# Kernel optimization log

Hardware: AMD Instinct MI355X
Metric: run time of the kernel (lower is better)

## Reference

```python
import jax, jax.numpy as jnp
import numpy as np

N = 6144
IN_DIM = 256
OUT_DIM = 256
NUM_HEADS = 4
HEAD_DIM = OUT_DIM // NUM_HEADS  # 64
NEG_SLOPE = 0.2


def setup_inputs() -> dict:
    key = jax.random.key(0)
    k_x, k_adj, k_W, k_a = jax.random.split(key, 4)
    x = jax.random.normal(k_x, (N, IN_DIM), dtype=jnp.float32)
    adj = jax.random.randint(k_adj, (N, N), 0, 2, dtype=jnp.int32)
    # nn.Linear(in_dim, out_dim, bias=False): store as [in_dim, out_dim] so y = x @ W
    W = jax.random.normal(k_W, (IN_DIM, OUT_DIM), dtype=jnp.float32) / np.sqrt(IN_DIM)
    # nn.Linear(2*head_dim, 1, bias=False): a single attention vector shared across heads
    a = jax.random.normal(k_a, (2 * HEAD_DIM,), dtype=jnp.float32) / np.sqrt(2 * HEAD_DIM)
    return {"x": x, "adj": adj, "W": W, "a": a}


def reference(x, adj, W, a):
    n = x.shape[0]
    Wh = (x @ W).reshape(n, NUM_HEADS, HEAD_DIM)  # (N, H, D)
    a_src, a_dst = a[:HEAD_DIM], a[HEAD_DIM:]
    # score[h,i,j] = leaky_relu(a_src . Wh[i,h] + a_dst . Wh[j,h])
    f_src = jnp.einsum('nhd,d->hn', Wh, a_src)  # (H, N)
    f_dst = jnp.einsum('nhd,d->hn', Wh, a_dst)  # (H, N)
    e = f_src[:, :, None] + f_dst[:, None, :]   # (H, N, N)
    e = jnp.where(e > 0, e, NEG_SLOPE * e)      # LeakyReLU(0.2)
    mask = (adj != 0)[None, :, :]               # (1, N, N)
    e = jnp.where(mask, e, -jnp.inf)
    alpha = jax.nn.softmax(e, axis=-1)          # (H, N, N)
    alpha = jnp.nan_to_num(alpha, nan=0.0)      # empty rows -> 0 (matches torch)
    # dropout: eval mode (identity)
    out = jnp.einsum('hij,jhd->ihd', alpha, Wh).reshape(n, OUT_DIM)
    return out
```

## Files before the change

### kernel.cpp

```cpp
#include <hip/hip_runtime.h>

#define NN 6144
#define SHIFTC (12.0f*1.4426950408889634f)
#define LOG2E 1.4426950408889634f

typedef float f32x4 __attribute__((ext_vector_type(4)));
typedef short short8 __attribute__((ext_vector_type(8)));
typedef int   i32x4 __attribute__((ext_vector_type(4)));

__device__ __forceinline__ float bf2f(unsigned short u){
  return __uint_as_float(((unsigned int)u)<<16);
}
__device__ __forceinline__ unsigned short f2bf(float f){
  unsigned int x = __float_as_uint(f);
  x += 0x7fffu + ((x>>16)&1u);
  return (unsigned short)(x>>16);
}

__global__ __launch_bounds__(256) void k_gemm(const float* __restrict__ x,
                                              const float* __restrict__ W,
                                              unsigned short* __restrict__ wht){
  __shared__ float sx[16*256];
  const int t = threadIdx.x;
  const int i0 = blockIdx.x * 16;
  {
    const int r = t >> 4, kc = t & 15;
    const float* src = x + (size_t)(i0 + r)*256 + kc*16;
    float* dst = sx + r*256 + kc*16;
#pragma unroll
    for (int q = 0; q < 4; ++q)
      *reinterpret_cast<f32x4*>(dst + 4*q) = *reinterpret_cast<const f32x4*>(src + 4*q);
  }
  __syncthreads();
  float acc[16];
#pragma unroll
  for (int r = 0; r < 16; ++r) acc[r] = 0.f;
  for (int k = 0; k < 256; k += 4) {
    const float w0 = W[(size_t)(k+0)*256 + t];
    const float w1 = W[(size_t)(k+1)*256 + t];
    const float w2 = W[(size_t)(k+2)*256 + t];
    const float w3 = W[(size_t)(k+3)*256 + t];
#pragma unroll
    for (int r = 0; r < 16; ++r) {
      f32x4 xv = *reinterpret_cast<const f32x4*>(sx + r*256 + k);
      acc[r] = fmaf(xv.x, w0, acc[r]);
      acc[r] = fmaf(xv.y, w1, acc[r]);
      acc[r] = fmaf(xv.z, w2, acc[r]);
      acc[r] = fmaf(xv.w, w3, acc[r]);
    }
  }
  alignas(16) unsigned short buf[16];
#pragma unroll
  for (int r = 0; r < 16; ++r) buf[r] = f2bf(acc[r]);
  unsigned short* dst = wht + (size_t)t*NN + i0;
  *reinterpret_cast<uint4*>(dst)     = *reinterpret_cast<const uint4*>(buf);
  *reinterpret_cast<uint4*>(dst + 8) = *reinterpret_cast<const uint4*>(buf + 8);
}

__global__ __launch_bounds__(256) void k_f(const unsigned short* __restrict__ wht,
                                           const float* __restrict__ a,
                                           float* __restrict__ fs2,
                                           float* __restrict__ edp,
                                           float* __restrict__ edn){
  __shared__ unsigned short sw[256*64];
  const int t = threadIdx.x;
  const int i0 = blockIdx.x * 64;
  {
    const unsigned short* src = wht + (size_t)t*NN + i0;
    unsigned short* dst = sw + t*64;
#pragma unroll
    for (int q = 0; q < 8; ++q)
      *reinterpret_cast<uint4*>(dst + q*8) = *reinterpret_cast<const uint4*>(src + q*8);
  }
  __syncthreads();
  const int ii = t & 63, h = t >> 6;
  float s_ = 0.f, d_ = 0.f;
#pragma unroll 16
  for (int d = 0; d < 64; ++d) {
    const float v = bf2f(sw[(h*64 + d)*64 + ii]);
    s_ = fmaf(v, a[d],      s_);
    d_ = fmaf(v, a[64 + d], d_);
  }
  const float fs2v = s_ * LOG2E;
  const float fd2v = d_ * LOG2E;
  fs2[(size_t)h*NN + i0 + ii] = fs2v;
  edp[(size_t)h*NN + i0 + ii] = exp2f(fd2v - SHIFTC);
  edn[(size_t)h*NN + i0 + ii] = exp2f(0.2f * fd2v);
}

__global__ __launch_bounds__(256) void k_attn(const int* __restrict__ adj,
                                              const unsigned short* __restrict__ wht,
                                              const float* __restrict__ fs2,
                                              const float* __restrict__ edp,
                                              const float* __restrict__ edn,
                                              float* __restrict__ apart,
                                              float* __restrict__ lpart,
                                              int nsteps){
  __shared__ unsigned short swht[2][64*72];
  __shared__ unsigned int   smask[2][128];
  __shared__ float          sedp[2][64];
  __shared__ float          sedn[2][64];
  const int t  = threadIdx.x;
  const int w  = t >> 6, l = t & 63, lr = l & 15, hi = l >> 4;
  const int bid = blockIdx.x;
  const int h   = (bid >> 3) & 3;
  const int g   = (bid & 7) | ((bid >> 5) << 3);
  const int it  = g % 96;
  const int js  = g / 96;
  const int i0 = it * 64;
  const int jbase = js * nsteps * 64;
  const int i_row = i0 + w*16 + lr;

  const float fsv  = fs2[(size_t)h*NN + i_row];
  const float EiNh = exp2f(-0.8f*fsv - SHIFTC);

  f32x4 acc[4];
#pragma unroll
  for (int q = 0; q < 4; ++q) acc[q] = (f32x4){0.f,0.f,0.f,0.f};
  float ls = 0.f;

  const int r_ = t >> 2, ch_ = t & 3;
  const int* asrc = adj + (size_t)(i0 + r_)*NN + jbase + ch_*16;
  const unsigned short* wsrc = wht + (size_t)(h*64 + r_)*NN + jbase + ch_*16;
  const float* pesrc = edp + (size_t)h*NN + jbase;
  const float* nesrc = edn + (size_t)h*NN + jbase;

  {
    i32x4 aj[4];
#pragma unroll
    for (int q = 0; q < 4; ++q) aj[q] = *reinterpret_cast<const i32x4*>(asrc + q*4);
    const uint4 wv0 = *reinterpret_cast<const uint4*>(wsrc);
    const uint4 wv1 = *reinterpret_cast<const uint4*>(wsrc + 8);
    unsigned int bits = 0u;
#pragma unroll
    for (int q = 0; q < 4; ++q) {
      bits |= ((unsigned)aj[q].x) << (q*4 + 0);
      bits |= ((unsigned)aj[q].y) << (q*4 + 1);
      bits |= ((unsigned)aj[q].z) << (q*4 + 2);
      bits |= ((unsigned)aj[q].w) << (q*4 + 3);
    }
    unsigned short* dst = &swht[0][r_*72 + ch_*16];
    *reinterpret_cast<uint4*>(dst)     = wv0;
    *reinterpret_cast<uint4*>(dst + 8) = wv1;
    reinterpret_cast<unsigned short*>(smask[0])[r_*4 + ch_] = (unsigned short)bits;
    if (t < 64) { sedp[0][t] = pesrc[t]; sedn[0][t] = nesrc[t]; }
  }
  __syncthreads();

  for (int st = 0; st < nsteps; ++st) {
    const int cur = st & 1, nxt = cur ^ 1;
    const bool pf = (st + 1) < nsteps;

    i32x4 ajp[4]; uint4 wvp0, wvp1; float pep = 0.f, nep = 0.f;
    if (pf) {
      const int o = (st + 1) * 64;
#pragma unroll
      for (int q = 0; q < 4; ++q)
        ajp[q] = *reinterpret_cast<const i32x4*>(asrc + o + q*4);
      wvp0 = *reinterpret_cast<const uint4*>(wsrc + o);
      wvp1 = *reinterpret_cast<const uint4*>(wsrc + o + 8);
      if (t < 64) { pep = pesrc[o + t]; nep = nesrc[o + t]; }
    }

    const unsigned int m0 = smask[cur][(w*16 + lr)*2 + 0];
    const unsigned int m1 = smask[cur][(w*16 + lr)*2 + 1];
    float maskf[16];
#pragma unroll
    for (int e = 0; e < 8; ++e) {
      maskf[e]     = ((m0 >> (8*hi + e)) & 1u) ? 1.f : 0.f;
      maskf[8 + e] = ((m1 >> (8*hi + e)) & 1u) ? 1.f : 0.f;
    }
    const f32x4 ep0 = *reinterpret_cast<const f32x4*>(&sedp[cur][8*hi + 0]);
    const f32x4 ep1 = *reinterpret_cast<const f32x4*>(&sedp[cur][8*hi + 4]);
    const f32x4 ep2 = *reinterpret_cast<const f32x4*>(&sedp[cur][32 + 8*hi + 0]);
    const f32x4 ep3 = *reinterpret_cast<const f32x4*>(&sedp[cur][32 + 8*hi + 4]);
    const f32x4 en0 = *reinterpret_cast<const f32x4*>(&sedn[cur][8*hi + 0]);
    const f32x4 en1 = *reinterpret_cast<const f32x4*>(&sedn[cur][8*hi + 4]);
    const f32x4 en2 = *reinterpret_cast<const f32x4*>(&sedn[cur][32 + 8*hi + 0]);
    const f32x4 en3 = *reinterpret_cast<const f32x4*>(&sedn[cur][32 + 8*hi + 4]);
    float p[16];
#pragma unroll
    for (int e = 0; e < 4; ++e) {
      p[e]      = maskf[e]      * fmaxf(ep0[e], EiNh * en0[e]);
      p[4 + e]  = maskf[4 + e]  * fmaxf(ep1[e], EiNh * en1[e]);
      p[8 + e]  = maskf[8 + e]  * fmaxf(ep2[e], EiNh * en2[e]);
      p[12 + e] = maskf[12 + e] * fmaxf(ep3[e], EiNh * en3[e]);
    }
    float lsh = 0.f;
#pragma unroll
    for (int e = 0; e < 16; ++e) lsh += p[e];
    ls += lsh;
    int4 aw0, aw1;
    asm("v_cvt_pk_bf16_f32 %0, %1, %2" : "=v"(aw0.x) : "v"(p[0]),  "v"(p[1]));
    asm("v_cvt_pk_bf16_f32 %0, %1, %2" : "=v"(aw0.y) : "v"(p[2]),  "v"(p[3]));
    asm("v_cvt_pk_bf16_f32 %0, %1, %2" : "=v"(aw0.z) : "v"(p[4]),  "v"(p[5]));
    asm("v_cvt_pk_bf16_f32 %0, %1, %2" : "=v"(aw0.w) : "v"(p[6]),  "v"(p[7]));
    asm("v_cvt_pk_bf16_f32 %0, %1, %2" : "=v"(aw1.x) : "v"(p[8]),  "v"(p[9]));
    asm("v_cvt_pk_bf16_f32 %0, %1, %2" : "=v"(aw1.y) : "v"(p[10]), "v"(p[11]));
    asm("v_cvt_pk_bf16_f32 %0, %1, %2" : "=v"(aw1.z) : "v"(p[12]), "v"(p[13]));
    asm("v_cvt_pk_bf16_f32 %0, %1, %2" : "=v"(aw1.w) : "v"(p[14]), "v"(p[15]));
    const short8 af0 = __builtin_bit_cast(short8, aw0);
    const short8 af1 = __builtin_bit_cast(short8, aw1);
#pragma unroll
    for (int nc = 0; nc < 4; ++nc) {
      const unsigned short* bp = &swht[cur][(nc*16 + lr)*72 + 8*hi];
      const short8 b0 = *reinterpret_cast<const short8*>(bp);
      const short8 b1 = *reinterpret_cast<const short8*>(bp + 32);
      acc[nc] = __builtin_amdgcn_mfma_f32_16x16x32_bf16(af0, b0, acc[nc], 0, 0, 0);
      acc[nc] = __builtin_amdgcn_mfma_f32_16x16x32_bf16(af1, b1, acc[nc], 0, 0, 0);
    }

    if (pf) {
      unsigned int bits = 0u;
#pragma unroll
      for (int q = 0; q < 4; ++q) {
        bits |= ((unsigned)ajp[q].x) << (q*4 + 0);
        bits |= ((unsigned)ajp[q].y) << (q*4 + 1);
        bits |= ((unsigned)ajp[q].z) << (q*4 + 2);
        bits |= ((unsigned)ajp[q].w) << (q*4 + 3);
      }
      unsigned short* dst = &swht[nxt][r_*72 + ch_*16];
      *reinterpret_cast<uint4*>(dst)     = wvp0;
      *reinterpret_cast<uint4*>(dst + 8) = wvp1;
      reinterpret_cast<unsigned short*>(smask[nxt])[r_*4 + ch_] = (unsigned short)bits;
      if (t < 64) { sedp[nxt][t] = pep; sedn[nxt][t] = nep; }
    }
    __syncthreads();
  }

  {
    float v = ls;
    v += __shfl_xor(v, 16, 64);
    v += __shfl_xor(v, 32, 64);
    ls = v;
  }
  if (hi == 0)
    lpart[((size_t)js*4 + h)*NN + i_row] = ls;
#pragma unroll
  for (int nc = 0; nc < 4; ++nc)
#pragma unroll
    for (int rg = 0; rg < 4; ++rg) {
      const int irow = i0 + w*16 + 4*hi + rg;
      const int col  = h*64 + nc*16 + lr;
      apart[((size_t)js*NN + irow)*256 + col] = acc[nc][rg];
    }
}

__global__ __launch_bounds__(256) void k_comb(const float* __restrict__ apart,
                                              const float* __restrict__ lpart,
                                              float* __restrict__ out,
                                              int jsplit){
  const int idx = blockIdx.x * 256 + threadIdx.x;
  const int i = idx >> 8, c = idx & 255, h = c >> 6;
  float num = 0.f, den = 0.f;
  for (int s = 0; s < jsplit; ++s) {
    num += apart[((size_t)s*NN + i)*256 + c];
    den += lpart[((size_t)s*4 + h)*NN + i];
  }
  out[idx] = (den > 0.f) ? (num / den) : 0.f;
}

extern "C" void kernel_launch(void* const* d_in, const int* in_sizes, int n_in,
                              void* d_out, int out_size, void* d_ws, size_t ws_size,
                              hipStream_t stream) {
  const float* x   = (const float*)d_in[0];
  const int*   adj = (const int*)d_in[1];
  const float* W   = (const float*)d_in[2];
  const float* a   = (const float*)d_in[3];
  float* out = (float*)d_out;
  char* ws = (char*)d_ws;

  size_t off = 0;
  unsigned short* wht = (unsigned short*)(ws + off); off += (size_t)256*NN*2;
  float* fs2 = (float*)(ws + off); off += (size_t)4*NN*4;
  float* edp = (float*)(ws + off); off += (size_t)4*NN*4;
  float* edn = (float*)(ws + off); off += (size_t)4*NN*4;

  int jsplit = 8;
  while (jsplit > 1 &&
         off + (size_t)jsplit*4*NN*4 + (size_t)jsplit*NN*256*4 > ws_size)
    jsplit >>= 1;

  float* lpart = (float*)(ws + off); off += (size_t)jsplit*4*NN*4;
  float* apart = (float*)(ws + off);

  const int nsteps = NN / (jsplit * 64);

  k_gemm<<<dim3(NN/16), dim3(256), 0, stream>>>(x, W, wht);
  k_f   <<<dim3(NN/64), dim3(256), 0, stream>>>(wht, a, fs2, edp, edn);
  k_attn<<<dim3(4*(NN/64)*jsplit), dim3(256), 0, stream>>>(adj, wht, fs2, edp, edn, apart, lpart, nsteps);
  k_comb<<<dim3((out_size + 255)/256), dim3(256), 0, stream>>>(apart, lpart, out, jsplit);
}
```

Baseline: 113.4 us.

## Prefetch adjacency two steps ahead and compute softmax denominator via MFMA

Restructures the main loop into a manually unrolled two-stage ping-pong. Adjacency loads are issued two steps ahead while the bf16 features and edge terms are loaded one step ahead, so global-load latency overlaps more MFMA work. The per-row sum of probabilities now comes from an extra MFMA against a ones vector instead of a scalar add chain and cross-lane shuffles. The edp/edn loads are also split across two thread groups. In exchange it uses more registers and two extra MFMAs per step, and the denominator is now summed from bf16-rounded values, matching the numerator.

```diff
diff --git a/kernel.cpp b/kernel.cpp
--- a/kernel.cpp
+++ b/kernel.cpp
@@ -117,7 +117,9 @@
   f32x4 acc[4];
 #pragma unroll
   for (int q = 0; q < 4; ++q) acc[q] = (f32x4){0.f,0.f,0.f,0.f};
-  float ls = 0.f;
+  f32x4 acc_den = (f32x4){0.f,0.f,0.f,0.f};
+  const short8 vones = { (short)0x3F80,(short)0x3F80,(short)0x3F80,(short)0x3F80,
+                         (short)0x3F80,(short)0x3F80,(short)0x3F80,(short)0x3F80 };
 
   const int r_ = t >> 2, ch_ = t & 3;
   const int* asrc = adj + (size_t)(i0 + r_)*NN + jbase + ch_*16;
@@ -125,50 +127,29 @@
   const float* pesrc = edp + (size_t)h*NN + jbase;
   const float* nesrc = edn + (size_t)h*NN + jbase;
 
-  {
-    i32x4 aj[4];
-#pragma unroll
-    for (int q = 0; q < 4; ++q) aj[q] = *reinterpret_cast<const i32x4*>(asrc + q*4);
-    const uint4 wv0 = *reinterpret_cast<const uint4*>(wsrc);
-    const uint4 wv1 = *reinterpret_cast<const uint4*>(wsrc + 8);
-    unsigned int bits = 0u;
-#pragma unroll
-    for (int q = 0; q < 4; ++q) {
-      bits |= ((unsigned)aj[q].x) << (q*4 + 0);
-      bits |= ((unsigned)aj[q].y) << (q*4 + 1);
-      bits |= ((unsigned)aj[q].z) << (q*4 + 2);
-      bits |= ((unsigned)aj[q].w) << (q*4 + 3);
-    }
-    unsigned short* dst = &swht[0][r_*72 + ch_*16];
-    *reinterpret_cast<uint4*>(dst)     = wv0;
-    *reinterpret_cast<uint4*>(dst + 8) = wv1;
-    reinterpret_cast<unsigned short*>(smask[0])[r_*4 + ch_] = (unsigned short)bits;
-    if (t < 64) { sedp[0][t] = pesrc[t]; sedn[0][t] = nesrc[t]; }
-  }
-  __syncthreads();
-
-  for (int st = 0; st < nsteps; ++st) {
-    const int cur = st & 1, nxt = cur ^ 1;
-    const bool pf = (st + 1) < nsteps;
-
-    i32x4 ajp[4]; uint4 wvp0, wvp1; float pep = 0.f, nep = 0.f;
-    if (pf) {
-      const int o = (st + 1) * 64;
-#pragma unroll
-      for (int q = 0; q < 4; ++q)
-        ajp[q] = *reinterpret_cast<const i32x4*>(asrc + o + q*4);
-      wvp0 = *reinterpret_cast<const uint4*>(wsrc + o);
-      wvp1 = *reinterpret_cast<const uint4*>(wsrc + o + 8);
-      if (t < 64) { pep = pesrc[o + t]; nep = nesrc[o + t]; }
-    }
-
+  auto commit = [&](int nxt, i32x4 A0, i32x4 A1, i32x4 A2, i32x4 A3,
+                    uint4 W0, uint4 W1, float PE, float NE) {
+    unsigned int bits =
+        ((unsigned)A0.x)       | (((unsigned)A0.y)<<1)  | (((unsigned)A0.z)<<2)  | (((unsigned)A0.w)<<3)  |
+        (((unsigned)A1.x)<<4)  | (((unsigned)A1.y)<<5)  | (((unsigned)A1.z)<<6)  | (((unsigned)A1.w)<<7)  |
+        (((unsigned)A2.x)<<8)  | (((unsigned)A2.y)<<9)  | (((unsigned)A2.z)<<10) | (((unsigned)A2.w)<<11) |
+        (((unsigned)A3.x)<<12) | (((unsigned)A3.y)<<13) | (((unsigned)A3.z)<<14) | (((unsigned)A3.w)<<15);
+    unsigned short* dst = &swht[nxt][r_*72 + ch_*16];
+    *reinterpret_cast<uint4*>(dst)     = W0;
+    *reinterpret_cast<uint4*>(dst + 8) = W1;
+    reinterpret_cast<unsigned short*>(smask[nxt])[r_*4 + ch_] = (unsigned short)bits;
+    if (t < 64)       sedp[nxt][t]      = PE;
+    else if (t < 128) sedn[nxt][t - 64] = NE;
+  };
+
+  auto compute_step = [&](int cur) {
     const unsigned int m0 = smask[cur][(w*16 + lr)*2 + 0];
     const unsigned int m1 = smask[cur][(w*16 + lr)*2 + 1];
     float maskf[16];
 #pragma unroll
     for (int e = 0; e < 8; ++e) {
-      maskf[e]     = ((m0 >> (8*hi + e)) & 1u) ? 1.f : 0.f;
-      maskf[8 + e] = ((m1 >> (8*hi + e)) & 1u) ? 1.f : 0.f;
+      maskf[e]     = (float)((m0 >> (8*hi + e)) & 1u);
+      maskf[8 + e] = (float)((m1 >> (8*hi + e)) & 1u);
     }
     const f32x4 ep0 = *reinterpret_cast<const f32x4*>(&sedp[cur][8*hi + 0]);
     const f32x4 ep1 = *reinterpret_cast<const f32x4*>(&sedp[cur][8*hi + 4]);
@@ -186,10 +167,6 @@
       p[8 + e]  = maskf[8 + e]  * fmaxf(ep2[e], EiNh * en2[e]);
       p[12 + e] = maskf[12 + e] * fmaxf(ep3[e], EiNh * en3[e]);
     }
-    float lsh = 0.f;
-#pragma unroll
-    for (int e = 0; e < 16; ++e) lsh += p[e];
-    ls += lsh;
     int4 aw0, aw1;
     asm("v_cvt_pk_bf16_f32 %0, %1, %2" : "=v"(aw0.x) : "v"(p[0]),  "v"(p[1]));
     asm("v_cvt_pk_bf16_f32 %0, %1, %2" : "=v"(aw0.y) : "v"(p[2]),  "v"(p[3]));
@@ -201,6 +178,8 @@
     asm("v_cvt_pk_bf16_f32 %0, %1, %2" : "=v"(aw1.w) : "v"(p[14]), "v"(p[15]));
     const short8 af0 = __builtin_bit_cast(short8, aw0);
     const short8 af1 = __builtin_bit_cast(short8, aw1);
+    acc_den = __builtin_amdgcn_mfma_f32_16x16x32_bf16(af0, vones, acc_den, 0, 0, 0);
+    acc_den = __builtin_amdgcn_mfma_f32_16x16x32_bf16(af1, vones, acc_den, 0, 0, 0);
 #pragma unroll
     for (int nc = 0; nc < 4; ++nc) {
       const unsigned short* bp = &swht[cur][(nc*16 + lr)*72 + 8*hi];
@@ -209,33 +188,73 @@
       acc[nc] = __builtin_amdgcn_mfma_f32_16x16x32_bf16(af0, b0, acc[nc], 0, 0, 0);
       acc[nc] = __builtin_amdgcn_mfma_f32_16x16x32_bf16(af1, b1, acc[nc], 0, 0, 0);
     }
-
-    if (pf) {
-      unsigned int bits = 0u;
-#pragma unroll
-      for (int q = 0; q < 4; ++q) {
-        bits |= ((unsigned)ajp[q].x) << (q*4 + 0);
-        bits |= ((unsigned)ajp[q].y) << (q*4 + 1);
-        bits |= ((unsigned)ajp[q].z) << (q*4 + 2);
-        bits |= ((unsigned)ajp[q].w) << (q*4 + 3);
-      }
-      unsigned short* dst = &swht[nxt][r_*72 + ch_*16];
-      *reinterpret_cast<uint4*>(dst)     = wvp0;
-      *reinterpret_cast<uint4*>(dst + 8) = wvp1;
-      reinterpret_cast<unsigned short*>(smask[nxt])[r_*4 + ch_] = (unsigned short)bits;
-      if (t < 64) { sedp[nxt][t] = pep; sedn[nxt][t] = nep; }
+  };
+
+  i32x4 ajA0, ajA1, ajA2, ajA3, ajB0, ajB1, ajB2, ajB3;
+  {
+    const i32x4 a0 = *reinterpret_cast<const i32x4*>(asrc + 0);
+    const i32x4 a1 = *reinterpret_cast<const i32x4*>(asrc + 4);
+    const i32x4 a2 = *reinterpret_cast<const i32x4*>(asrc + 8);
+    const i32x4 a3 = *reinterpret_cast<const i32x4*>(asrc + 12);
+    const uint4 w0 = *reinterpret_cast<const uint4*>(wsrc);
+    const uint4 w1 = *reinterpret_cast<const uint4*>(wsrc + 8);
+    const float pe = (t < 64) ? pesrc[t] : 0.f;
+    const float ne = (t >= 64 && t < 128) ? nesrc[t - 64] : 0.f;
+    commit(0, a0, a1, a2, a3, w0, w1, pe, ne);
+  }
+  if (nsteps > 1) {
+    const int* an = asrc + 64;
+    ajA0 = *reinterpret_cast<const i32x4*>(an + 0);
+    ajA1 = *reinterpret_cast<const i32x4*>(an + 4);
+    ajA2 = *reinterpret_cast<const i32x4*>(an + 8);
+    ajA3 = *reinterpret_cast<const i32x4*>(an + 12);
+  }
+  __syncthreads();
+
+  for (int st = 0; st < nsteps; st += 2) {
+    if (st + 2 < nsteps) {
+      const int* an = asrc + (st + 2)*64;
+      ajB0 = *reinterpret_cast<const i32x4*>(an + 0);
+      ajB1 = *reinterpret_cast<const i32x4*>(an + 4);
+      ajB2 = *reinterpret_cast<const i32x4*>(an + 8);
+      ajB3 = *reinterpret_cast<const i32x4*>(an + 12);
+    }
+    {
+      const int o = (st + 1)*64;
+      const uint4 wv0 = *reinterpret_cast<const uint4*>(wsrc + o);
+      const uint4 wv1 = *reinterpret_cast<const uint4*>(wsrc + o + 8);
+      const float pe = (t < 64) ? pesrc[o + t] : 0.f;
+      const float ne = (t >= 64 && t < 128) ? nesrc[o + t - 64] : 0.f;
+      compute_step(0);
+      commit(1, ajA0, ajA1, ajA2, ajA3, wv0, wv1, pe, ne);
     }
     __syncthreads();
-  }
-
-  {
-    float v = ls;
-    v += __shfl_xor(v, 16, 64);
-    v += __shfl_xor(v, 32, 64);
-    ls = v;
-  }
-  if (hi == 0)
-    lpart[((size_t)js*4 + h)*NN + i_row] = ls;
+    if (st + 3 < nsteps) {
+      const int* an = asrc + (st + 3)*64;
+      ajA0 = *reinterpret_cast<const i32x4*>(an + 0);
+      ajA1 = *reinterpret_cast<const i32x4*>(an + 4);
+      ajA2 = *reinterpret_cast<const i32x4*>(an + 8);
+      ajA3 = *reinterpret_cast<const i32x4*>(an + 12);
+    }
+    if (st + 2 < nsteps) {
+      const int o = (st + 2)*64;
+      const uint4 wv0 = *reinterpret_cast<const uint4*>(wsrc + o);
+      const uint4 wv1 = *reinterpret_cast<const uint4*>(wsrc + o + 8);
+      const float pe = (t < 64) ? pesrc[o + t] : 0.f;
+      const float ne = (t >= 64 && t < 128) ? nesrc[o + t - 64] : 0.f;
+      compute_step(1);
+      commit(0, ajB0, ajB1, ajB2, ajB3, wv0, wv1, pe, ne);
+    } else {
+      compute_step(1);
+    }
+    __syncthreads();
+  }
+
+  if (lr == 0) {
+#pragma unroll
+    for (int rg = 0; rg < 4; ++rg)
+      lpart[((size_t)js*4 + h)*NN + i0 + w*16 + 4*hi + rg] = acc_den[rg];
+  }
 #pragma unroll
   for (int nc = 0; nc < 4; ++nc)
 #pragma unroll
```

Result: slower. 128.1 us (+12.9%).

## Widen attention j-tile to 128 with two wave groups and LDS reduction

Applied to the files above, without the earlier changes.

The attention kernel now uses 512 threads per block and processes a 128-wide j tile each step. Two groups of four waves each handle half of the columns and combine their partial accumulators and row sums through shared memory at the end. This halves the number of loop iterations and block-wide barriers per block and gives more waves to hide memory latency. In exchange it uses more LDS and registers per block, which may lower occupancy, and it adds a reduction pass at the end.

```diff
diff --git a/kernel.cpp b/kernel.cpp
--- a/kernel.cpp
+++ b/kernel.cpp
@@ -1,6 +1,8 @@
 #include <hip/hip_runtime.h>
 
 #define NN 6144
+#define BK 128
+#define WPAD 136
 #define SHIFTC (12.0f*1.4426950408889634f)
 #define LOG2E 1.4426950408889634f
 
@@ -88,7 +90,7 @@
   edn[(size_t)h*NN + i0 + ii] = exp2f(0.2f * fd2v);
 }
 
-__global__ __launch_bounds__(256) void k_attn(const int* __restrict__ adj,
+__global__ __launch_bounds__(512) void k_attn(const int* __restrict__ adj,
                                               const unsigned short* __restrict__ wht,
                                               const float* __restrict__ fs2,
                                               const float* __restrict__ edp,
@@ -96,20 +98,22 @@
                                               float* __restrict__ apart,
                                               float* __restrict__ lpart,
                                               int nsteps){
-  __shared__ unsigned short swht[2][64*72];
-  __shared__ unsigned int   smask[2][128];
-  __shared__ float          sedp[2][64];
-  __shared__ float          sedn[2][64];
+  __shared__ unsigned short swht[2][64*WPAD];
+  __shared__ unsigned int   smask[2][256];
+  __shared__ float          sedp[2][BK];
+  __shared__ float          sedn[2][BK];
   const int t  = threadIdx.x;
-  const int w  = t >> 6, l = t & 63, lr = l & 15, hi = l >> 4;
+  const int w8 = t >> 6, l = t & 63, lr = l & 15, hi = l >> 4;
+  const int ww = w8 & 3;
+  const int jh = w8 >> 2;
   const int bid = blockIdx.x;
   const int h   = (bid >> 3) & 3;
   const int g   = (bid & 7) | ((bid >> 5) << 3);
   const int it  = g % 96;
   const int js  = g / 96;
   const int i0 = it * 64;
-  const int jbase = js * nsteps * 64;
-  const int i_row = i0 + w*16 + lr;
+  const int jbase = js * nsteps * BK;
+  const int i_row = i0 + ww*16 + lr;
 
   const float fsv  = fs2[(size_t)h*NN + i_row];
   const float EiNh = exp2f(-0.8f*fsv - SHIFTC);
@@ -119,7 +123,7 @@
   for (int q = 0; q < 4; ++q) acc[q] = (f32x4){0.f,0.f,0.f,0.f};
   float ls = 0.f;
 
-  const int r_ = t >> 2, ch_ = t & 3;
+  const int r_ = t >> 3, ch_ = t & 7;
   const int* asrc = adj + (size_t)(i0 + r_)*NN + jbase + ch_*16;
   const unsigned short* wsrc = wht + (size_t)(h*64 + r_)*NN + jbase + ch_*16;
   const float* pesrc = edp + (size_t)h*NN + jbase;
@@ -139,11 +143,12 @@
       bits |= ((unsigned)aj[q].z) << (q*4 + 2);
       bits |= ((unsigned)aj[q].w) << (q*4 + 3);
     }
-    unsigned short* dst = &swht[0][r_*72 + ch_*16];
+    unsigned short* dst = &swht[0][r_*WPAD + ch_*16];
     *reinterpret_cast<uint4*>(dst)     = wv0;
     *reinterpret_cast<uint4*>(dst + 8) = wv1;
-    reinterpret_cast<unsigned short*>(smask[0])[r_*4 + ch_] = (unsigned short)bits;
-    if (t < 64) { sedp[0][t] = pesrc[t]; sedn[0][t] = nesrc[t]; }
+    reinterpret_cast<unsigned short*>(smask[0])[r_*8 + ch_] = (unsigned short)bits;
+    if (t < BK)          sedp[0][t]      = pesrc[t];
+    else if (t < 2*BK)   sedn[0][t - BK] = nesrc[t - BK];
   }
   __syncthreads();
 
@@ -153,31 +158,34 @@
 
     i32x4 ajp[4]; uint4 wvp0, wvp1; float pep = 0.f, nep = 0.f;
     if (pf) {
-      const int o = (st + 1) * 64;
+      const int o = (st + 1) * BK;
 #pragma unroll
       for (int q = 0; q < 4; ++q)
         ajp[q] = *reinterpret_cast<const i32x4*>(asrc + o + q*4);
       wvp0 = *reinterpret_cast<const uint4*>(wsrc + o);
       wvp1 = *reinterpret_cast<const uint4*>(wsrc + o + 8);
-      if (t < 64) { pep = pesrc[o + t]; nep = nesrc[o + t]; }
-    }
-
-    const unsigned int m0 = smask[cur][(w*16 + lr)*2 + 0];
-    const unsigned int m1 = smask[cur][(w*16 + lr)*2 + 1];
+      if (t < BK)        pep = pesrc[o + t];
+      else if (t < 2*BK) nep = nesrc[o + t - BK];
+    }
+
+    const int row = ww*16 + lr;
+    const unsigned int m0 = smask[cur][row*4 + jh*2 + 0];
+    const unsigned int m1 = smask[cur][row*4 + jh*2 + 1];
     float maskf[16];
 #pragma unroll
     for (int e = 0; e < 8; ++e) {
-      maskf[e]     = ((m0 >> (8*hi + e)) & 1u) ? 1.f : 0.f;
-      maskf[8 + e] = ((m1 >> (8*hi + e)) & 1u) ? 1.f : 0.f;
-    }
-    const f32x4 ep0 = *reinterpret_cast<const f32x4*>(&sedp[cur][8*hi + 0]);
-    const f32x4 ep1 = *reinterpret_cast<const f32x4*>(&sedp[cur][8*hi + 4]);
-    const f32x4 ep2 = *reinterpret_cast<const f32x4*>(&sedp[cur][32 + 8*hi + 0]);
-    const f32x4 ep3 = *reinterpret_cast<const f32x4*>(&sedp[cur][32 + 8*hi + 4]);
-    const f32x4 en0 = *reinterpret_cast<const f32x4*>(&sedn[cur][8*hi + 0]);
-    const f32x4 en1 = *reinterpret_cast<const f32x4*>(&sedn[cur][8*hi + 4]);
-    const f32x4 en2 = *reinterpret_cast<const f32x4*>(&sedn[cur][32 + 8*hi + 0]);
-    const f32x4 en3 = *reinterpret_cast<const f32x4*>(&sedn[cur][32 + 8*hi + 4]);
+      maskf[e]     = (float)((m0 >> (8*hi + e)) & 1u);
+      maskf[8 + e] = (float)((m1 >> (8*hi + e)) & 1u);
+    }
+    const int jo = jh*64;
+    const f32x4 ep0 = *reinterpret_cast<const f32x4*>(&sedp[cur][jo + 8*hi + 0]);
+    const f32x4 ep1 = *reinterpret_cast<const f32x4*>(&sedp[cur][jo + 8*hi + 4]);
+    const f32x4 ep2 = *reinterpret_cast<const f32x4*>(&sedp[cur][jo + 32 + 8*hi + 0]);
+    const f32x4 ep3 = *reinterpret_cast<const f32x4*>(&sedp[cur][jo + 32 + 8*hi + 4]);
+    const f32x4 en0 = *reinterpret_cast<const f32x4*>(&sedn[cur][jo + 8*hi + 0]);
+    const f32x4 en1 = *reinterpret_cast<const f32x4*>(&sedn[cur][jo + 8*hi + 4]);
+    const f32x4 en2 = *reinterpret_cast<const f32x4*>(&sedn[cur][jo + 32 + 8*hi + 0]);
+    const f32x4 en3 = *reinterpret_cast<const f32x4*>(&sedn[cur][jo + 32 + 8*hi + 4]);
     float p[16];
 #pragma unroll
     for (int e = 0; e < 4; ++e) {
@@ -203,7 +211,7 @@
     const short8 af1 = __builtin_bit_cast(short8, aw1);
 #pragma unroll
     for (int nc = 0; nc < 4; ++nc) {
-      const unsigned short* bp = &swht[cur][(nc*16 + lr)*72 + 8*hi];
+      const unsigned short* bp = &swht[cur][(nc*16 + lr)*WPAD + jo + 8*hi];
       const short8 b0 = *reinterpret_cast<const short8*>(bp);
       const short8 b1 = *reinterpret_cast<const short8*>(bp + 32);
       acc[nc] = __builtin_amdgcn_mfma_f32_16x16x32_bf16(af0, b0, acc[nc], 0, 0, 0);
@@ -219,31 +227,52 @@
         bits |= ((unsigned)ajp[q].z) << (q*4 + 2);
         bits |= ((unsigned)ajp[q].w) << (q*4 + 3);
       }
-      unsigned short* dst = &swht[nxt][r_*72 + ch_*16];
+      unsigned short* dst = &swht[nxt][r_*WPAD + ch_*16];
       *reinterpret_cast<uint4*>(dst)     = wvp0;
       *reinterpret_cast<uint4*>(dst + 8) = wvp1;
-      reinterpret_cast<unsigned short*>(smask[nxt])[r_*4 + ch_] = (unsigned short)bits;
-      if (t < 64) { sedp[nxt][t] = pep; sedn[nxt][t] = nep; }
+      reinterpret_cast<unsigned short*>(smask[nxt])[r_*8 + ch_] = (unsigned short)bits;
+      if (t < BK)        sedp[nxt][t]      = pep;
+      else if (t < 2*BK) sedn[nxt][t - BK] = nep;
     }
     __syncthreads();
   }
 
-  {
-    float v = ls;
-    v += __shfl_xor(v, 16, 64);
-    v += __shfl_xor(v, 32, 64);
-    ls = v;
-  }
-  if (hi == 0)
-    lpart[((size_t)js*4 + h)*NN + i_row] = ls;
-#pragma unroll
-  for (int nc = 0; nc < 4; ++nc)
-#pragma unroll
-    for (int rg = 0; rg < 4; ++rg) {
-      const int irow = i0 + w*16 + 4*hi + rg;
-      const int col  = h*64 + nc*16 + lr;
-      apart[((size_t)js*NN + irow)*256 + col] = acc[nc][rg];
-    }
+  float* scr = reinterpret_cast<float*>(swht);
+  const int sbase = (ww*64 + l) * 17;
+  if (jh == 1) {
+#pragma unroll
+    for (int nc = 0; nc < 4; ++nc)
+#pragma unroll
+      for (int rg = 0; rg < 4; ++rg)
+        scr[sbase + nc*4 + rg] = acc[nc][rg];
+    scr[sbase + 16] = ls;
+  }
+  __syncthreads();
+  if (jh == 0) {
+#pragma unroll
+    for (int nc = 0; nc < 4; ++nc)
+#pragma unroll
+      for (int rg = 0; rg < 4; ++rg)
+        acc[nc][rg] += scr[sbase + nc*4 + rg];
+    ls += scr[sbase + 16];
+
+    {
+      float v = ls;
+      v += __shfl_xor(v, 16, 64);
+      v += __shfl_xor(v, 32, 64);
+      ls = v;
+    }
+    if (hi == 0)
+      lpart[((size_t)js*4 + h)*NN + i_row] = ls;
+#pragma unroll
+    for (int nc = 0; nc < 4; ++nc)
+#pragma unroll
+      for (int rg = 0; rg < 4; ++rg) {
+        const int irow = i0 + ww*16 + 4*hi + rg;
+        const int col  = h*64 + nc*16 + lr;
+        apart[((size_t)js*NN + irow)*256 + col] = acc[nc][rg];
+      }
+  }
 }
 
 __global__ __launch_bounds__(256) void k_comb(const float* __restrict__ apart,
@@ -284,10 +313,10 @@
   float* lpart = (float*)(ws + off); off += (size_t)jsplit*4*NN*4;
   float* apart = (float*)(ws + off);
 
-  const int nsteps = NN / (jsplit * 64);
+  const int nsteps = NN / (jsplit * BK);
 
   k_gemm<<<dim3(NN/16), dim3(256), 0, stream>>>(x, W, wht);
   k_f   <<<dim3(NN/64), dim3(256), 0, stream>>>(wht, a, fs2, edp, edn);
-  k_attn<<<dim3(4*(NN/64)*jsplit), dim3(256), 0, stream>>>(adj, wht, fs2, edp, edn, apart, lpart, nsteps);
+  k_attn<<<dim3(4*(NN/64)*jsplit), dim3(512), 0, stream>>>(adj, wht, fs2, edp, edn, apart, lpart, nsteps);
   k_comb<<<dim3((out_size + 255)/256), dim3(256), 0, stream>>>(apart, lpart, out, jsplit);
 }
```

Result: slower. 126.2 us (+11.3%).
